# Performance work log

Measured on AMD Instinct MI355X. Metric: run time of the kernel, lower is better.

Reference implementation:

```python
import jax, jax.numpy as jnp
import numpy as np

DIM = 128
NUM_HEADS = 8
HEAD_DIM = DIM // NUM_HEADS
SCALE = HEAD_DIM ** -0.5


def _attn_branch(xs, Wq, bq, Wp, bp):
    # xs: (N, L, C) batch of sequences; Q=K=V=q (per the module)
    N, L, C = xs.shape
    q = xs @ Wq + bq                                   # (N, L, C)
    q = q.reshape(N, L, NUM_HEADS, HEAD_DIM).transpose(0, 2, 1, 3)  # (N, h, L, d)
    qs = q * SCALE
    attn = jax.nn.softmax(jnp.einsum('nhld,nhmd->nhlm', qs, qs), axis=-1)
    out = jnp.einsum('nhlm,nhmd->nhld', attn, q)       # (N, h, L, d)
    out = out.transpose(0, 2, 1, 3).reshape(N, L, C)
    return out @ Wp + bp


def setup_inputs() -> dict:
    key = jax.random.key(0)
    ks = jax.random.split(key, 12)
    B, C, D, H, W = 1, DIM, 31, 32, 32
    s = 0.02
    return {
        'x': jax.random.normal(ks[0], (B, C, D, H, W), jnp.float32),
        'Wq_spec': jax.random.normal(ks[1], (C, C), jnp.float32) * s,
        'bq_spec': jnp.zeros((C,), jnp.float32),
        'Wp_spec': jax.random.normal(ks[2], (C, C), jnp.float32) * s,
        'bp_spec': jnp.zeros((C,), jnp.float32),
        'Wq_spat': jax.random.normal(ks[3], (C, C), jnp.float32) * s,
        'bq_spat': jnp.zeros((C,), jnp.float32),
        'Wp_spat': jax.random.normal(ks[4], (C, C), jnp.float32) * s,
        'bp_spat': jnp.zeros((C,), jnp.float32),
        'Wg': jax.random.normal(ks[5], (2 * C, C), jnp.float32) * s,
        'bg': jnp.zeros((C,), jnp.float32),
    }


def reference(x, Wq_spec, bq_spec, Wp_spec, bp_spec,
              Wq_spat, bq_spat, Wp_spat, bp_spat, Wg, bg):
    B, C, D, H, W = x.shape
    # ---- spectral branch: sequences of length D per spatial position ----
    x_spec = x.transpose(0, 3, 4, 2, 1).reshape(B * H * W, D, C)
    out_spec = _attn_branch(x_spec, Wq_spec, bq_spec, Wp_spec, bp_spec)
    out_spectral = out_spec.reshape(B, H, W, D, C).transpose(0, 4, 3, 1, 2)  # (B,C,D,H,W)
    # ---- spatial branch: sequences of length H*W per band ----
    x_spat = x.transpose(0, 2, 3, 4, 1).reshape(B * D, H * W, C)
    out_spat = _attn_branch(x_spat, Wq_spat, bq_spat, Wp_spat, bp_spat)
    out_spatial = out_spat.reshape(B, D, H, W, C).transpose(0, 4, 1, 2, 3)   # (B,C,D,H,W)
    # ---- sigmoid-gated fusion (global average pooled gate) ----
    gi = jnp.concatenate([
        out_spectral.mean(axis=(2, 3, 4)),
        out_spatial.mean(axis=(2, 3, 4)),
    ], axis=-1)                                          # (B, 2C)
    gate = jax.nn.sigmoid(gi @ Wg + bg)[:, :, None, None, None]  # (B,C,1,1,1)
    return gate * out_spectral + (1.0 - gate) * out_spatial
```

## Files before the change

kernel.cpp:

```cpp
#include <hip/hip_runtime.h>
#include <cstddef>

#define CC 128
#define NH 8
#define HD 16
#define DDIM 31
#define HWW 1024
#define TOK 31744
#define SCALE2 0.0625f
#define QTOK 64

typedef __attribute__((ext_vector_type(4))) short  short4v;
typedef __attribute__((ext_vector_type(8))) short  short8v;
typedef __attribute__((ext_vector_type(4))) float  float4v;
typedef __attribute__((ext_vector_type(2))) unsigned uint2v;
typedef __attribute__((ext_vector_type(8))) __bf16 bf16x8;

__device__ inline unsigned bf16rne(float f) {
    unsigned u = __float_as_uint(f);
    return (u + 0x7fffu + ((u >> 16) & 1u)) >> 16;
}
__device__ inline float bf2f(unsigned h) { return __uint_as_float(h << 16); }

__device__ inline unsigned packsplit(float v) {
    unsigned h = bf16rne(v);
    unsigned l = bf16rne(v - bf2f(h));
    return h | (l << 16);
}
__device__ inline uint2 pack_hi4(uint4 p) {
    return make_uint2((p.x & 0xffffu) | (p.y << 16),
                      (p.z & 0xffffu) | (p.w << 16));
}
__device__ inline uint2 pack_lo4(uint4 p) {
    return make_uint2((p.x >> 16) | (p.y & 0xffff0000u),
                      (p.z >> 16) | (p.w & 0xffff0000u));
}

__device__ inline short4v pack_pf(unsigned u0, unsigned u1,
                                  unsigned u2, unsigned u3) {
    uint2v pd;
    pd[0] = __builtin_amdgcn_perm(u1, u0, 0x07060302u);
    pd[1] = __builtin_amdgcn_perm(u3, u2, 0x07060302u);
    return __builtin_bit_cast(short4v, pd);
}

__device__ inline float4v mfma32(short8v a, short8v b, float4v c) {
    return __builtin_amdgcn_mfma_f32_16x16x32_bf16(
        __builtin_bit_cast(bf16x8, a), __builtin_bit_cast(bf16x8, b), c, 0, 0, 0);
}

__device__ inline void load_wfrags32(const float* __restrict__ W, int co0, int l,
                                     int quad, short8v* ah, short8v* al)
{
#pragma unroll
    for (int k4 = 0; k4 < 4; ++k4) {
#pragma unroll
        for (int j = 0; j < 8; ++j) {
            float w = W[(size_t)(k4 * 32 + quad * 8 + j) * CC + co0 + l];
            unsigned h = bf16rne(w);
            ah[k4][j] = (short)h;
            al[k4][j] = (short)bf16rne(w - bf2f(h));
        }
    }
}

#define AST 136

__global__ __launch_bounds__(512, 4) void qproj_kernel(
    const float* __restrict__ x,
    const float* __restrict__ Wq1, const float* __restrict__ Wq2,
    const float* __restrict__ bq1, const float* __restrict__ bq2,
    unsigned* __restrict__ q1p, unsigned* __restrict__ q2p,
    float* __restrict__ sums)
{
    __shared__ ushort sbuf[2 * QTOK * AST];
    ushort* Ahi = sbuf;
    ushort* Alo = sbuf + QTOK * AST;
    unsigned* S = (unsigned*)sbuf;
    const int tid = threadIdx.x;
    const int t0  = blockIdx.x * QTOK;
    if (blockIdx.x == 0 && tid < 2 * CC) sums[tid] = 0.f;

    for (int i = tid; i < CC * QTOK / 4; i += 512) {
        int t4 = i & 15, ci = i >> 4;
        float4 v = *(const float4*)&x[(size_t)ci * TOK + t0 + t4 * 4];
        float xv[4] = {v.x, v.y, v.z, v.w};
#pragma unroll
        for (int e = 0; e < 4; ++e) {
            unsigned h = bf16rne(xv[e]);
            unsigned lw = bf16rne(xv[e] - bf2f(h));
            Ahi[(t4 * 4 + e) * AST + ci] = (ushort)h;
            Alo[(t4 * 4 + e) * AST + ci] = (ushort)lw;
        }
    }
    __syncthreads();

    const int lane = tid & 63;
    const int l    = lane & 15;
    const int quad = lane >> 4;
    const int co0  = (tid >> 6) * 16;

    short8v ah[2][4], al[2][4];
    load_wfrags32(Wq1, co0, l, quad, ah[0], al[0]);
    load_wfrags32(Wq2, co0, l, quad, ah[1], al[1]);
    float4v acc[2][4];
#pragma unroll
    for (int br = 0; br < 2; ++br)
#pragma unroll
        for (int nt = 0; nt < 4; ++nt) acc[br][nt] = (float4v){0.f, 0.f, 0.f, 0.f};
#pragma unroll
    for (int k4 = 0; k4 < 4; ++k4) {
#pragma unroll
        for (int nt = 0; nt < 4; ++nt) {
            short8v bh = *(const short8v*)&Ahi[(nt * 16 + l) * AST + k4 * 32 + quad * 8];
            short8v bl = *(const short8v*)&Alo[(nt * 16 + l) * AST + k4 * 32 + quad * 8];
            acc[0][nt] = mfma32(ah[0][k4], bh, acc[0][nt]);
            acc[0][nt] = mfma32(ah[0][k4], bl, acc[0][nt]);
            acc[0][nt] = mfma32(al[0][k4], bh, acc[0][nt]);
            acc[1][nt] = mfma32(ah[1][k4], bh, acc[1][nt]);
            acc[1][nt] = mfma32(ah[1][k4], bl, acc[1][nt]);
            acc[1][nt] = mfma32(al[1][k4], bh, acc[1][nt]);
        }
    }

    for (int branch = 0; branch < 2; ++branch) {
        const float* bq = branch ? bq2 : bq1;
        unsigned* op    = branch ? q2p : q1p;
        float4 bv = *(const float4*)&bq[co0 + quad * 4];
        float bb[4] = {bv.x, bv.y, bv.z, bv.w};
        __syncthreads();
#pragma unroll
        for (int nt = 0; nt < 4; ++nt) {
#pragma unroll
            for (int reg = 0; reg < 4; ++reg)
                S[(nt * 16 + l) * AST + co0 + quad * 4 + reg] =
                    packsplit(acc[branch][nt][reg] + bb[reg]);
        }
        __syncthreads();
        for (int i = tid; i < QTOK * 32; i += 512) {
            int t = i >> 5, c4 = i & 31;
            uint4 pv = *(const uint4*)&S[t * AST + c4 * 4];
            *(uint4*)&op[(size_t)(t0 + t) * CC + c4 * 4] = pv;
        }
    }
}

#define QS2 132
#define QSS 20
#define QTP 1044
__global__ __launch_bounds__(1024, 4) void attn_kernel(
    unsigned* __restrict__ q1p, unsigned* __restrict__ q2p,
    float* __restrict__ sums)
{
    __shared__ __align__(16) ushort smem[HWW * QSS + HD * QTP];
    __shared__ float fsum[CC];
    const int tid  = threadIdx.x;
    const int lane = tid & 63;
    const int l    = lane & 15;
    const int quad = lane >> 4;
    const float k2 = SCALE2 * 1.44269504f;
    const short4v onesb = {(short)0x3F80, (short)0x3F80, (short)0x3F80, (short)0x3F80};
    if (tid < CC) fsum[tid] = 0.f;

    {
        const int d = blockIdx.x >> 3, h = blockIdx.x & 7;
        ushort* Qs  = smem;
        ushort* QTs = smem + HWW * QSS;
        const size_t base = (size_t)d * HWW * CC + h * HD;

        for (int i = tid; i < HWW * 4; i += 1024) {
            int row = i >> 2, q4 = i & 3;
            uint4 p = *(const uint4*)&q2p[base + (size_t)row * CC + q4 * 4];
            *(uint2*)&Qs[row * QSS + q4 * 4] = pack_hi4(p);
            QTs[(q4 * 4 + 0) * QTP + row] = (ushort)p.x;
            QTs[(q4 * 4 + 1) * QTP + row] = (ushort)p.y;
            QTs[(q4 * 4 + 2) * QTP + row] = (ushort)p.z;
            QTs[(q4 * 4 + 3) * QTP + row] = (ushort)p.w;
        }
        __syncthreads();

        const int Rw = (tid >> 6) * 64;
        short4v qf[4];
#pragma unroll
        for (int lt = 0; lt < 4; ++lt) {
            short4v raw = *(short4v*)&Qs[(Rw + lt * 16 + l) * QSS + quad * 4];
            short4v sc;
#pragma unroll
            for (int e = 0; e < 4; ++e) {
                float f = bf2f((unsigned)(ushort)raw[e]) * k2;
                sc[e] = (short)bf16rne(f);
            }
            qf[lt] = sc;
        }

        float4v acc[4], accs[4];
#pragma unroll
        for (int lt = 0; lt < 4; ++lt) {
            acc[lt]  = (float4v){0.f, 0.f, 0.f, 0.f};
            accs[lt] = (float4v){0.f, 0.f, 0.f, 0.f};
        }

#pragma unroll 2
        for (int mt = 0; mt < 64; ++mt) {
            const int m0 = mt * 16;
            short4v ka = *(short4v*)&Qs[(m0 + l) * QSS + quad * 4];
            short4v vb = *(short4v*)&QTs[l * QTP + m0 + quad * 4];
#pragma unroll
            for (int lt = 0; lt < 4; ++lt) {
                float4v s = __builtin_amdgcn_mfma_f32_16x16x16bf16_1k(
                    ka, qf[lt], (float4v){0.f, 0.f, 0.f, 0.f}, 0, 0, 0);
                unsigned u0 = __float_as_uint(__builtin_amdgcn_exp2f(s[0]));
                unsigned u1 = __float_as_uint(__builtin_amdgcn_exp2f(s[1]));
                unsigned u2 = __float_as_uint(__builtin_amdgcn_exp2f(s[2]));
                unsigned u3 = __float_as_uint(__builtin_amdgcn_exp2f(s[3]));
                short4v pf = pack_pf(u0, u1, u2, u3);
                acc[lt]  = __builtin_amdgcn_mfma_f32_16x16x16bf16_1k(vb, pf, acc[lt], 0, 0, 0);
                accs[lt] = __builtin_amdgcn_mfma_f32_16x16x16bf16_1k(onesb, pf, accs[lt], 0, 0, 0);
            }
        }

        float vsum[4] = {0.f, 0.f, 0.f, 0.f};
#pragma unroll
        for (int lt = 0; lt < 4; ++lt) {
            float inv = 1.f / accs[lt][0];
            int token = Rw + lt * 16 + l;
            float v0 = acc[lt][0] * inv, v1 = acc[lt][1] * inv;
            float v2 = acc[lt][2] * inv, v3 = acc[lt][3] * inv;
            uint4 pv;
            pv.x = packsplit(v0); pv.y = packsplit(v1);
            pv.z = packsplit(v2); pv.w = packsplit(v3);
            *(uint4*)&q2p[base + (size_t)token * CC + quad * 4] = pv;
            vsum[0] += v0; vsum[1] += v1; vsum[2] += v2; vsum[3] += v3;
        }
#pragma unroll
        for (int reg = 0; reg < 4; ++reg) {
            float v = vsum[reg];
            v += __shfl_xor(v, 1); v += __shfl_xor(v, 2);
            v += __shfl_xor(v, 4); v += __shfl_xor(v, 8);
            if (l == 0) atomicAdd(&fsum[quad * 4 + reg], v);
        }
        __syncthreads();
        if (tid < HD) atomicAdd(&sums[CC + h * HD + tid], fsum[tid]);
    }

    const int half_id = blockIdx.x >> 1;
    const bool has_job = (blockIdx.x & 1) ? (half_id < 4) : (half_id < 124);
    if (!has_job) return;
    const int job = (blockIdx.x & 1) ? (124 + half_id) : half_id;
    const int hw0 = job * 8;

    __syncthreads();
    if (tid < CC) fsum[tid] = 0.f;

    const int wave = tid >> 6;
    const int hwl  = wave >> 1;
    const int half = wave & 1;
    const int hw   = hw0 + hwl;
    ushort* Q = smem + hwl * (32 * QS2);
    for (int it = 0; it < 8; ++it) {
        int idx = it * 64 + lane;
        int dd = half * 16 + (idx >> 5), c4 = idx & 31;
        if (dd < 31) {
            uint4 p = *(const uint4*)&q1p[((size_t)dd * HWW + hw) * CC + c4 * 4];
            *(uint2*)&Q[dd * QS2 + c4 * 4] = pack_hi4(p);
        }
    }
    if (half) for (int i = lane; i < 128; i += 64) Q[31 * QS2 + i] = 0;
    __syncthreads();

    const int hh = half * 4;
#pragma unroll
    for (int hl = 0; hl < 4; ++hl) {
        const int hc = (hh + hl) * HD;
        short4v qf[2];
        qf[0] = *(const short4v*)&Q[l * QS2 + hc + quad * 4];
        qf[1] = *(const short4v*)&Q[(16 + l) * QS2 + hc + quad * 4];
        short4v va[2];
#pragma unroll
        for (int j = 0; j < 2; ++j)
#pragma unroll
            for (int jj = 0; jj < 4; ++jj)
                va[j][jj] = (short)Q[(j * 16 + quad * 4 + jj) * QS2 + hc + l];

        float4v o[2]   = {(float4v){0.f,0.f,0.f,0.f}, (float4v){0.f,0.f,0.f,0.f}};
        float4v osr[2] = {(float4v){0.f,0.f,0.f,0.f}, (float4v){0.f,0.f,0.f,0.f}};
#pragma unroll
        for (int j = 0; j < 2; ++j) {
#pragma unroll
            for (int i2 = 0; i2 < 2; ++i2) {
                float4v s = __builtin_amdgcn_mfma_f32_16x16x16bf16_1k(
                    qf[j], qf[i2], (float4v){0.f,0.f,0.f,0.f}, 0, 0, 0);
                unsigned u0 = __float_as_uint(__builtin_amdgcn_exp2f(s[0] * k2));
                unsigned u1 = __float_as_uint(__builtin_amdgcn_exp2f(s[1] * k2));
                unsigned u2 = __float_as_uint(__builtin_amdgcn_exp2f(s[2] * k2));
                unsigned u3 = __float_as_uint(__builtin_amdgcn_exp2f(s[3] * k2));
                if (j == 1 && quad == 3) u3 = 0;
                short4v pf = pack_pf(u0, u1, u2, u3);
                o[i2]   = __builtin_amdgcn_mfma_f32_16x16x16bf16_1k(va[j], pf, o[i2], 0, 0, 0);
                osr[i2] = __builtin_amdgcn_mfma_f32_16x16x16bf16_1k(onesb, pf, osr[i2], 0, 0, 0);
            }
        }
        float vsum[4] = {0.f, 0.f, 0.f, 0.f};
#pragma unroll
        for (int i2 = 0; i2 < 2; ++i2) {
            float inv = 1.f / osr[i2][0];
            int dq = i2 * 16 + l;
            if (dq < 31) {
                uint4 pv;
                float v0 = o[i2][0] * inv, v1 = o[i2][1] * inv;
                float v2 = o[i2][2] * inv, v3 = o[i2][3] * inv;
                pv.x = packsplit(v0); pv.y = packsplit(v1);
                pv.z = packsplit(v2); pv.w = packsplit(v3);
                *(uint4*)&q1p[((size_t)dq * HWW + hw) * CC + hc + quad * 4] = pv;
                vsum[0] += v0; vsum[1] += v1; vsum[2] += v2; vsum[3] += v3;
            }
        }
#pragma unroll
        for (int r = 0; r < 4; ++r) {
            float v = vsum[r];
            v += __shfl_xor(v, 1); v += __shfl_xor(v, 2);
            v += __shfl_xor(v, 4); v += __shfl_xor(v, 8);
            if (l == 0) atomicAdd(&fsum[hc + quad * 4 + r], v);
        }
    }
    __syncthreads();
    if (tid < CC) atomicAdd(&sums[tid], fsum[tid]);
}

__global__ __launch_bounds__(512, 4) void oproj_kernel(
    const unsigned* __restrict__ q1p, const unsigned* __restrict__ q2p,
    const float* __restrict__ Wp1, const float* __restrict__ Wp2,
    const float* __restrict__ bp1, const float* __restrict__ bp2,
    const float* __restrict__ Wg,  const float* __restrict__ bg,
    const float* __restrict__ sums, float* __restrict__ out)
{
    __shared__ ushort sbuf[2 * 64 * AST];
    ushort* Ahi = sbuf;
    ushort* Alo = sbuf + 64 * AST;
    unsigned* S = (unsigned*)sbuf;
    __shared__ float pa[4][CC];
    __shared__ float giv[2 * CC];
    __shared__ float gf[CC];
    const int tid = threadIdx.x;
    const int t0  = blockIdx.x * 64;
    const int lane = tid & 63;
    const int l    = lane & 15;
    const int quad = lane >> 4;
    const int co0  = (tid >> 6) * 16;

    {
        const int part = tid >> 7, c = tid & 127;
        const float* Wp = (part < 2) ? Wp1 : Wp2;
        const float* sp = (part < 2) ? sums : sums + CC;
        const int k0 = (part & 1) * 64;
        float a = 0.f;
        for (int kk = 0; kk < 64; ++kk) {
            int k = k0 + kk;
            a += sp[k] * Wp[(size_t)k * CC + c];
        }
        pa[part][c] = a;
        __syncthreads();
        if (tid < 2 * CC) {
            float m = (tid < CC) ? (pa[0][tid] + pa[1][tid])
                                 : (pa[2][tid - CC] + pa[3][tid - CC]);
            float bb = (tid < CC) ? bp1[tid] : bp2[tid - CC];
            giv[tid] = m * (1.f / (float)TOK) + bb;
        }
        __syncthreads();
        float b = 0.f;
        for (int kk = 0; kk < 64; ++kk) {
            int j = part * 64 + kk;
            b += giv[j] * Wg[(size_t)j * CC + c];
        }
        pa[part][c] = b;
        __syncthreads();
        if (tid < CC)
            gf[tid] = 1.f / (1.f + __expf(-(bg[tid] + pa[0][tid] + pa[1][tid] +
                                           pa[2][tid] + pa[3][tid])));
    }

    float4v acc[2][4];
#pragma unroll
    for (int br = 0; br < 2; ++br)
#pragma unroll
        for (int nt = 0; nt < 4; ++nt) acc[br][nt] = (float4v){0.f, 0.f, 0.f, 0.f};

    for (int br = 0; br < 2; ++br) {
        const unsigned* Ap = br ? q2p : q1p;
        const float*    W  = br ? Wp2 : Wp1;
        short8v ah[4], al[4];
        load_wfrags32(W, co0, l, quad, ah, al);
        __syncthreads();
        for (int i = tid; i < 64 * 32; i += 512) {
            int t = i >> 5, c4 = i & 31;
            uint4 p = *(const uint4*)&Ap[(size_t)(t0 + t) * CC + c4 * 4];
            *(uint2*)&Ahi[t * AST + c4 * 4] = pack_hi4(p);
            *(uint2*)&Alo[t * AST + c4 * 4] = pack_lo4(p);
        }
        __syncthreads();
#pragma unroll
        for (int k4 = 0; k4 < 4; ++k4) {
#pragma unroll
            for (int nt = 0; nt < 4; ++nt) {
                short8v bh = *(const short8v*)&Ahi[(nt * 16 + l) * AST + k4 * 32 + quad * 8];
                short8v bl = *(const short8v*)&Alo[(nt * 16 + l) * AST + k4 * 32 + quad * 8];
                acc[br][nt] = mfma32(ah[k4], bh, acc[br][nt]);
                acc[br][nt] = mfma32(ah[k4], bl, acc[br][nt]);
                acc[br][nt] = mfma32(al[k4], bh, acc[br][nt]);
            }
        }
    }

    float4 b1 = *(const float4*)&bp1[co0 + quad * 4];
    float4 b2 = *(const float4*)&bp2[co0 + quad * 4];
    float bb1[4] = {b1.x, b1.y, b1.z, b1.w};
    float bb2[4] = {b2.x, b2.y, b2.z, b2.w};
    float gg[4];
#pragma unroll
    for (int e = 0; e < 4; ++e) gg[e] = gf[co0 + quad * 4 + e];

    __syncthreads();
#pragma unroll
    for (int nt = 0; nt < 4; ++nt) {
        int tl = nt * 16 + l;
#pragma unroll
        for (int reg = 0; reg < 4; ++reg) {
            float v = gg[reg] * (acc[0][nt][reg] + bb1[reg]) +
                      (1.f - gg[reg]) * (acc[1][nt][reg] + bb2[reg]);
            S[(co0 + quad * 4 + reg) * 66 + tl] = __float_as_uint(v);
        }
    }
    __syncthreads();
    for (int i = tid; i < 128 * 32; i += 512) {
        int co = i >> 5, t2 = i & 31;
        uint2 v = *(const uint2*)&S[co * 66 + t2 * 2];
        *(uint2*)&out[(size_t)co * TOK + t0 + t2 * 2] = v;
    }
}

extern "C" void kernel_launch(void* const* d_in, const int* in_sizes, int n_in,
                              void* d_out, int out_size, void* d_ws, size_t ws_size,
                              hipStream_t stream)
{
    const float* x   = (const float*)d_in[0];
    const float* Wq1 = (const float*)d_in[1];
    const float* bq1 = (const float*)d_in[2];
    const float* Wp1 = (const float*)d_in[3];
    const float* bp1 = (const float*)d_in[4];
    const float* Wq2 = (const float*)d_in[5];
    const float* bq2 = (const float*)d_in[6];
    const float* Wp2 = (const float*)d_in[7];
    const float* bp2 = (const float*)d_in[8];
    const float* Wg  = (const float*)d_in[9];
    const float* bg  = (const float*)d_in[10];
    float* out = (float*)d_out;

    const size_t plane = (size_t)TOK * CC;
    unsigned* q1p = (unsigned*)d_ws;
    unsigned* q2p = q1p + plane;
    float*   sums = (float*)(q2p + plane);

    qproj_kernel<<<dim3(TOK / QTOK), 512, 0, stream>>>(x, Wq1, Wq2, bq1, bq2,
                                                       q1p, q2p, sums);
    attn_kernel<<<dim3(248), 1024, 0, stream>>>(q1p, q2p, sums);
    oproj_kernel<<<dim3(496), 512, 0, stream>>>(q1p, q2p,
                                                Wp1, Wp2, bp1, bp2, Wg, bg,
                                                sums, out);
}
```

Before: 173.0 us.

## Use 16x16x32 bf16 MFMA for PV and row-sum, coalesce x staging

Both attention kernels now compute two 16-key score tiles and pack the exponentials into an 8-element bf16 fragment. The PV product and the softmax row-sum then run as single K=32 MFMAs instead of pairs of K=16 MFMAs, which halves the accumulation instruction count. The qproj staging loop is also reorganised so each thread loads scalar x values along the token dimension and writes packed 4-channel uint2 words to LDS instead of scattered ushort stores. The trade-off is higher register pressure from keeping two score tiles live, plus a reliance on the K-slot mapping of the 16x16x32 MFMA lining up with the concatenated fragments.

```diff
diff --git a/kernel.cpp b/kernel.cpp
--- a/kernel.cpp
+++ b/kernel.cpp
@@ -14,6 +14,7 @@
 typedef __attribute__((ext_vector_type(8))) short  short8v;
 typedef __attribute__((ext_vector_type(4))) float  float4v;
 typedef __attribute__((ext_vector_type(2))) unsigned uint2v;
+typedef __attribute__((ext_vector_type(4))) unsigned uint4v;
 typedef __attribute__((ext_vector_type(8))) __bf16 bf16x8;
 
 __device__ inline unsigned bf16rne(float f) {
@@ -36,17 +37,24 @@
                       (p.z >> 16) | (p.w & 0xffff0000u));
 }
 
-__device__ inline short4v pack_pf(unsigned u0, unsigned u1,
-                                  unsigned u2, unsigned u3) {
-    uint2v pd;
+__device__ inline short8v pack_pf8(unsigned u0, unsigned u1, unsigned u2,
+                                   unsigned u3, unsigned u4, unsigned u5,
+                                   unsigned u6, unsigned u7) {
+    uint4v pd;
     pd[0] = __builtin_amdgcn_perm(u1, u0, 0x07060302u);
     pd[1] = __builtin_amdgcn_perm(u3, u2, 0x07060302u);
-    return __builtin_bit_cast(short4v, pd);
+    pd[2] = __builtin_amdgcn_perm(u5, u4, 0x07060302u);
+    pd[3] = __builtin_amdgcn_perm(u7, u6, 0x07060302u);
+    return __builtin_bit_cast(short8v, pd);
 }
 
 __device__ inline float4v mfma32(short8v a, short8v b, float4v c) {
     return __builtin_amdgcn_mfma_f32_16x16x32_bf16(
         __builtin_bit_cast(bf16x8, a), __builtin_bit_cast(bf16x8, b), c, 0, 0, 0);
+}
+__device__ inline float4v mfma16(short4v a, short4v b) {
+    return __builtin_amdgcn_mfma_f32_16x16x16bf16_1k(
+        a, b, (float4v){0.f, 0.f, 0.f, 0.f}, 0, 0, 0);
 }
 
 __device__ inline void load_wfrags32(const float* __restrict__ W, int co0, int l,
@@ -81,17 +89,25 @@
     const int t0  = blockIdx.x * QTOK;
     if (blockIdx.x == 0 && tid < 2 * CC) sums[tid] = 0.f;
 
-    for (int i = tid; i < CC * QTOK / 4; i += 512) {
-        int t4 = i & 15, ci = i >> 4;
-        float4 v = *(const float4*)&x[(size_t)ci * TOK + t0 + t4 * 4];
-        float xv[4] = {v.x, v.y, v.z, v.w};
-#pragma unroll
-        for (int e = 0; e < 4; ++e) {
-            unsigned h = bf16rne(xv[e]);
-            unsigned lw = bf16rne(xv[e] - bf2f(h));
-            Ahi[(t4 * 4 + e) * AST + ci] = (ushort)h;
-            Alo[(t4 * 4 + e) * AST + ci] = (ushort)lw;
-        }
+    for (int i = tid; i < QTOK * 32; i += 512) {
+        int t = i & 63, c4 = i >> 6;
+        unsigned hw[2], lw[2];
+#pragma unroll
+        for (int p = 0; p < 2; ++p) {
+            unsigned h0, l0, h1, l1;
+            {
+                float v = x[(size_t)(c4 * 4 + p * 2 + 0) * TOK + t0 + t];
+                h0 = bf16rne(v); l0 = bf16rne(v - bf2f(h0));
+            }
+            {
+                float v = x[(size_t)(c4 * 4 + p * 2 + 1) * TOK + t0 + t];
+                h1 = bf16rne(v); l1 = bf16rne(v - bf2f(h1));
+            }
+            hw[p] = h0 | (h1 << 16);
+            lw[p] = l0 | (l1 << 16);
+        }
+        *(uint2*)&Ahi[t * AST + c4 * 4] = make_uint2(hw[0], hw[1]);
+        *(uint2*)&Alo[t * AST + c4 * 4] = make_uint2(lw[0], lw[1]);
     }
     __syncthreads();
 
@@ -159,7 +175,8 @@
     const int l    = lane & 15;
     const int quad = lane >> 4;
     const float k2 = SCALE2 * 1.44269504f;
-    const short4v onesb = {(short)0x3F80, (short)0x3F80, (short)0x3F80, (short)0x3F80};
+    const short8v ones8 = {(short)0x3F80, (short)0x3F80, (short)0x3F80, (short)0x3F80,
+                           (short)0x3F80, (short)0x3F80, (short)0x3F80, (short)0x3F80};
     if (tid < CC) fsum[tid] = 0.f;
 
     {
@@ -200,22 +217,28 @@
             accs[lt] = (float4v){0.f, 0.f, 0.f, 0.f};
         }
 
-#pragma unroll 2
-        for (int mt = 0; mt < 64; ++mt) {
-            const int m0 = mt * 16;
-            short4v ka = *(short4v*)&Qs[(m0 + l) * QSS + quad * 4];
-            short4v vb = *(short4v*)&QTs[l * QTP + m0 + quad * 4];
+        for (int mt2 = 0; mt2 < 32; ++mt2) {
+            const int m0 = mt2 * 32;
+            short4v ka0 = *(short4v*)&Qs[(m0 + l) * QSS + quad * 4];
+            short4v ka1 = *(short4v*)&Qs[(m0 + 16 + l) * QSS + quad * 4];
+            short4v v0  = *(short4v*)&QTs[l * QTP + m0 + quad * 4];
+            short4v v1  = *(short4v*)&QTs[l * QTP + m0 + 16 + quad * 4];
+            short8v vb  = __builtin_shufflevector(v0, v1, 0, 1, 2, 3, 4, 5, 6, 7);
 #pragma unroll
             for (int lt = 0; lt < 4; ++lt) {
-                float4v s = __builtin_amdgcn_mfma_f32_16x16x16bf16_1k(
-                    ka, qf[lt], (float4v){0.f, 0.f, 0.f, 0.f}, 0, 0, 0);
-                unsigned u0 = __float_as_uint(__builtin_amdgcn_exp2f(s[0]));
-                unsigned u1 = __float_as_uint(__builtin_amdgcn_exp2f(s[1]));
-                unsigned u2 = __float_as_uint(__builtin_amdgcn_exp2f(s[2]));
-                unsigned u3 = __float_as_uint(__builtin_amdgcn_exp2f(s[3]));
-                short4v pf = pack_pf(u0, u1, u2, u3);
-                acc[lt]  = __builtin_amdgcn_mfma_f32_16x16x16bf16_1k(vb, pf, acc[lt], 0, 0, 0);
-                accs[lt] = __builtin_amdgcn_mfma_f32_16x16x16bf16_1k(onesb, pf, accs[lt], 0, 0, 0);
+                float4v s0 = mfma16(ka0, qf[lt]);
+                float4v s1 = mfma16(ka1, qf[lt]);
+                unsigned u0 = __float_as_uint(__builtin_amdgcn_exp2f(s0[0]));
+                unsigned u1 = __float_as_uint(__builtin_amdgcn_exp2f(s0[1]));
+                unsigned u2 = __float_as_uint(__builtin_amdgcn_exp2f(s0[2]));
+                unsigned u3 = __float_as_uint(__builtin_amdgcn_exp2f(s0[3]));
+                unsigned u4 = __float_as_uint(__builtin_amdgcn_exp2f(s1[0]));
+                unsigned u5 = __float_as_uint(__builtin_amdgcn_exp2f(s1[1]));
+                unsigned u6 = __float_as_uint(__builtin_amdgcn_exp2f(s1[2]));
+                unsigned u7 = __float_as_uint(__builtin_amdgcn_exp2f(s1[3]));
+                short8v pf = pack_pf8(u0, u1, u2, u3, u4, u5, u6, u7);
+                acc[lt]  = mfma32(vb, pf, acc[lt]);
+                accs[lt] = mfma32(ones8, pf, accs[lt]);
             }
         }
 
@@ -275,30 +298,31 @@
         short4v qf[2];
         qf[0] = *(const short4v*)&Q[l * QS2 + hc + quad * 4];
         qf[1] = *(const short4v*)&Q[(16 + l) * QS2 + hc + quad * 4];
-        short4v va[2];
-#pragma unroll
-        for (int j = 0; j < 2; ++j)
-#pragma unroll
-            for (int jj = 0; jj < 4; ++jj)
-                va[j][jj] = (short)Q[(j * 16 + quad * 4 + jj) * QS2 + hc + l];
+        short8v va8;
+#pragma unroll
+        for (int jj = 0; jj < 4; ++jj) {
+            va8[jj]     = (short)Q[(quad * 4 + jj) * QS2 + hc + l];
+            va8[jj + 4] = (short)Q[(16 + quad * 4 + jj) * QS2 + hc + l];
+        }
 
         float4v o[2]   = {(float4v){0.f,0.f,0.f,0.f}, (float4v){0.f,0.f,0.f,0.f}};
         float4v osr[2] = {(float4v){0.f,0.f,0.f,0.f}, (float4v){0.f,0.f,0.f,0.f}};
 #pragma unroll
-        for (int j = 0; j < 2; ++j) {
-#pragma unroll
-            for (int i2 = 0; i2 < 2; ++i2) {
-                float4v s = __builtin_amdgcn_mfma_f32_16x16x16bf16_1k(
-                    qf[j], qf[i2], (float4v){0.f,0.f,0.f,0.f}, 0, 0, 0);
-                unsigned u0 = __float_as_uint(__builtin_amdgcn_exp2f(s[0] * k2));
-                unsigned u1 = __float_as_uint(__builtin_amdgcn_exp2f(s[1] * k2));
-                unsigned u2 = __float_as_uint(__builtin_amdgcn_exp2f(s[2] * k2));
-                unsigned u3 = __float_as_uint(__builtin_amdgcn_exp2f(s[3] * k2));
-                if (j == 1 && quad == 3) u3 = 0;
-                short4v pf = pack_pf(u0, u1, u2, u3);
-                o[i2]   = __builtin_amdgcn_mfma_f32_16x16x16bf16_1k(va[j], pf, o[i2], 0, 0, 0);
-                osr[i2] = __builtin_amdgcn_mfma_f32_16x16x16bf16_1k(onesb, pf, osr[i2], 0, 0, 0);
-            }
+        for (int i2 = 0; i2 < 2; ++i2) {
+            float4v s0 = mfma16(qf[0], qf[i2]);
+            float4v s1 = mfma16(qf[1], qf[i2]);
+            unsigned u0 = __float_as_uint(__builtin_amdgcn_exp2f(s0[0] * k2));
+            unsigned u1 = __float_as_uint(__builtin_amdgcn_exp2f(s0[1] * k2));
+            unsigned u2 = __float_as_uint(__builtin_amdgcn_exp2f(s0[2] * k2));
+            unsigned u3 = __float_as_uint(__builtin_amdgcn_exp2f(s0[3] * k2));
+            unsigned u4 = __float_as_uint(__builtin_amdgcn_exp2f(s1[0] * k2));
+            unsigned u5 = __float_as_uint(__builtin_amdgcn_exp2f(s1[1] * k2));
+            unsigned u6 = __float_as_uint(__builtin_amdgcn_exp2f(s1[2] * k2));
+            unsigned u7 = __float_as_uint(__builtin_amdgcn_exp2f(s1[3] * k2));
+            if (quad == 3) u7 = 0;
+            short8v pf = pack_pf8(u0, u1, u2, u3, u4, u5, u6, u7);
+            o[i2]   = mfma32(va8, pf, o[i2]);
+            osr[i2] = mfma32(ones8, pf, osr[i2]);
         }
         float vsum[4] = {0.f, 0.f, 0.f, 0.f};
 #pragma unroll
```

Measured after the change: 170.4 us. About the same (-1.5%).

## Precompute split-bf16 weight planes and hoist gate computation into separate kernels

Applied to the files above, without the earlier changes.

Adds a prep kernel that converts the four projection weight matrices once into hi/lo bf16 planes in the workspace. The qproj and oproj blocks then load MFMA fragments with vector loads instead of each block doing strided fp32 loads and conversions. The sigmoid gate, previously recomputed redundantly by all 496 oproj blocks, moves to a single-block kernel, and the x staging loop in qproj is restructured to write packed pairs to LDS. The cost is two extra kernel launches and a serial dependency on the one-block gate kernel.

```diff
diff --git a/kernel.cpp b/kernel.cpp
--- a/kernel.cpp
+++ b/kernel.cpp
@@ -49,26 +49,53 @@
         __builtin_bit_cast(bf16x8, a), __builtin_bit_cast(bf16x8, b), c, 0, 0, 0);
 }
 
-__device__ inline void load_wfrags32(const float* __restrict__ W, int co0, int l,
-                                     int quad, short8v* ah, short8v* al)
-{
+#define AST 136
+#define WPL (CC * CC)
+
+__global__ __launch_bounds__(256) void wprep_kernel(
+    const float* __restrict__ Wq1, const float* __restrict__ Wq2,
+    const float* __restrict__ Wp1, const float* __restrict__ Wp2,
+    ushort* __restrict__ wplanes)
+{
+    const int m = blockIdx.x >> 4;
+    const int e = (blockIdx.x & 15) * 256 + threadIdx.x;
+    const int co = e >> 5, kb = e & 31;
+    const float* W = (m == 0) ? Wq1 : (m == 1) ? Wq2 : (m == 2) ? Wp1 : Wp2;
+    ushort* hi = wplanes + (size_t)m * 2 * WPL;
+    ushort* lo = hi + WPL;
+    ushort hv[4], lv[4];
+#pragma unroll
+    for (int j = 0; j < 4; ++j) {
+        float w = W[(size_t)(kb * 4 + j) * CC + co];
+        unsigned h = bf16rne(w);
+        hv[j] = (ushort)h;
+        lv[j] = (ushort)bf16rne(w - bf2f(h));
+    }
+    *(uint2*)&hi[(size_t)co * CC + kb * 4] =
+        make_uint2((unsigned)hv[0] | ((unsigned)hv[1] << 16),
+                   (unsigned)hv[2] | ((unsigned)hv[3] << 16));
+    *(uint2*)&lo[(size_t)co * CC + kb * 4] =
+        make_uint2((unsigned)lv[0] | ((unsigned)lv[1] << 16),
+                   (unsigned)lv[2] | ((unsigned)lv[3] << 16));
+}
+
+__device__ inline void load_wfrags_p(const ushort* __restrict__ Whi,
+                                     const ushort* __restrict__ Wlo,
+                                     int co0, int l, int quad,
+                                     short8v* ah, short8v* al)
+{
+    const ushort* rh = Whi + (size_t)(co0 + l) * CC + quad * 8;
+    const ushort* rl = Wlo + (size_t)(co0 + l) * CC + quad * 8;
 #pragma unroll
     for (int k4 = 0; k4 < 4; ++k4) {
-#pragma unroll
-        for (int j = 0; j < 8; ++j) {
-            float w = W[(size_t)(k4 * 32 + quad * 8 + j) * CC + co0 + l];
-            unsigned h = bf16rne(w);
-            ah[k4][j] = (short)h;
-            al[k4][j] = (short)bf16rne(w - bf2f(h));
-        }
-    }
-}
-
-#define AST 136
+        ah[k4] = *(const short8v*)&rh[k4 * 32];
+        al[k4] = *(const short8v*)&rl[k4 * 32];
+    }
+}
 
 __global__ __launch_bounds__(512, 4) void qproj_kernel(
     const float* __restrict__ x,
-    const float* __restrict__ Wq1, const float* __restrict__ Wq2,
+    const ushort* __restrict__ wplanes,
     const float* __restrict__ bq1, const float* __restrict__ bq2,
     unsigned* __restrict__ q1p, unsigned* __restrict__ q2p,
     float* __restrict__ sums)
@@ -81,17 +108,25 @@
     const int t0  = blockIdx.x * QTOK;
     if (blockIdx.x == 0 && tid < 2 * CC) sums[tid] = 0.f;
 
-    for (int i = tid; i < CC * QTOK / 4; i += 512) {
-        int t4 = i & 15, ci = i >> 4;
-        float4 v = *(const float4*)&x[(size_t)ci * TOK + t0 + t4 * 4];
-        float xv[4] = {v.x, v.y, v.z, v.w};
-#pragma unroll
-        for (int e = 0; e < 4; ++e) {
-            unsigned h = bf16rne(xv[e]);
-            unsigned lw = bf16rne(xv[e] - bf2f(h));
-            Ahi[(t4 * 4 + e) * AST + ci] = (ushort)h;
-            Alo[(t4 * 4 + e) * AST + ci] = (ushort)lw;
-        }
+    for (int i = tid; i < QTOK * 32; i += 512) {
+        int t = i & 63, c4 = i >> 6;
+        unsigned hw[2], lw[2];
+#pragma unroll
+        for (int p = 0; p < 2; ++p) {
+            unsigned h0, l0, h1, l1;
+            {
+                float v = x[(size_t)(c4 * 4 + p * 2 + 0) * TOK + t0 + t];
+                h0 = bf16rne(v); l0 = bf16rne(v - bf2f(h0));
+            }
+            {
+                float v = x[(size_t)(c4 * 4 + p * 2 + 1) * TOK + t0 + t];
+                h1 = bf16rne(v); l1 = bf16rne(v - bf2f(h1));
+            }
+            hw[p] = h0 | (h1 << 16);
+            lw[p] = l0 | (l1 << 16);
+        }
+        *(uint2*)&Ahi[t * AST + c4 * 4] = make_uint2(hw[0], hw[1]);
+        *(uint2*)&Alo[t * AST + c4 * 4] = make_uint2(lw[0], lw[1]);
     }
     __syncthreads();
 
@@ -101,8 +136,8 @@
     const int co0  = (tid >> 6) * 16;
 
     short8v ah[2][4], al[2][4];
-    load_wfrags32(Wq1, co0, l, quad, ah[0], al[0]);
-    load_wfrags32(Wq2, co0, l, quad, ah[1], al[1]);
+    load_wfrags_p(wplanes,           wplanes + WPL,     co0, l, quad, ah[0], al[0]);
+    load_wfrags_p(wplanes + 2 * WPL, wplanes + 3 * WPL, co0, l, quad, ah[1], al[1]);
     float4v acc[2][4];
 #pragma unroll
     for (int br = 0; br < 2; ++br)
@@ -327,20 +362,55 @@
     if (tid < CC) atomicAdd(&sums[tid], fsum[tid]);
 }
 
-__global__ __launch_bounds__(512, 4) void oproj_kernel(
-    const unsigned* __restrict__ q1p, const unsigned* __restrict__ q2p,
+__global__ __launch_bounds__(512) void gate_kernel(
     const float* __restrict__ Wp1, const float* __restrict__ Wp2,
     const float* __restrict__ bp1, const float* __restrict__ bp2,
     const float* __restrict__ Wg,  const float* __restrict__ bg,
-    const float* __restrict__ sums, float* __restrict__ out)
+    const float* __restrict__ sums, float* __restrict__ gfp)
+{
+    __shared__ float pa[4][CC];
+    __shared__ float giv[2 * CC];
+    const int tid = threadIdx.x;
+    const int part = tid >> 7, c = tid & 127;
+    const float* Wp = (part < 2) ? Wp1 : Wp2;
+    const float* sp = (part < 2) ? sums : sums + CC;
+    const int k0 = (part & 1) * 64;
+    float a = 0.f;
+    for (int kk = 0; kk < 64; ++kk) {
+        int k = k0 + kk;
+        a += sp[k] * Wp[(size_t)k * CC + c];
+    }
+    pa[part][c] = a;
+    __syncthreads();
+    if (tid < 2 * CC) {
+        float m = (tid < CC) ? (pa[0][tid] + pa[1][tid])
+                             : (pa[2][tid - CC] + pa[3][tid - CC]);
+        float bb = (tid < CC) ? bp1[tid] : bp2[tid - CC];
+        giv[tid] = m * (1.f / (float)TOK) + bb;
+    }
+    __syncthreads();
+    float b = 0.f;
+    for (int kk = 0; kk < 64; ++kk) {
+        int j = part * 64 + kk;
+        b += giv[j] * Wg[(size_t)j * CC + c];
+    }
+    pa[part][c] = b;
+    __syncthreads();
+    if (tid < CC)
+        gfp[tid] = 1.f / (1.f + __expf(-(bg[tid] + pa[0][tid] + pa[1][tid] +
+                                        pa[2][tid] + pa[3][tid])));
+}
+
+__global__ __launch_bounds__(512, 4) void oproj_kernel(
+    const unsigned* __restrict__ q1p, const unsigned* __restrict__ q2p,
+    const ushort* __restrict__ wplanes,
+    const float* __restrict__ bp1, const float* __restrict__ bp2,
+    const float* __restrict__ gfp, float* __restrict__ out)
 {
     __shared__ ushort sbuf[2 * 64 * AST];
     ushort* Ahi = sbuf;
     ushort* Alo = sbuf + 64 * AST;
     unsigned* S = (unsigned*)sbuf;
-    __shared__ float pa[4][CC];
-    __shared__ float giv[2 * CC];
-    __shared__ float gf[CC];
     const int tid = threadIdx.x;
     const int t0  = blockIdx.x * 64;
     const int lane = tid & 63;
@@ -348,37 +418,6 @@
     const int quad = lane >> 4;
     const int co0  = (tid >> 6) * 16;
 
-    {
-        const int part = tid >> 7, c = tid & 127;
-        const float* Wp = (part < 2) ? Wp1 : Wp2;
-        const float* sp = (part < 2) ? sums : sums + CC;
-        const int k0 = (part & 1) * 64;
-        float a = 0.f;
-        for (int kk = 0; kk < 64; ++kk) {
-            int k = k0 + kk;
-            a += sp[k] * Wp[(size_t)k * CC + c];
-        }
-        pa[part][c] = a;
-        __syncthreads();
-        if (tid < 2 * CC) {
-            float m = (tid < CC) ? (pa[0][tid] + pa[1][tid])
-                                 : (pa[2][tid - CC] + pa[3][tid - CC]);
-            float bb = (tid < CC) ? bp1[tid] : bp2[tid - CC];
-            giv[tid] = m * (1.f / (float)TOK) + bb;
-        }
-        __syncthreads();
-        float b = 0.f;
-        for (int kk = 0; kk < 64; ++kk) {
-            int j = part * 64 + kk;
-            b += giv[j] * Wg[(size_t)j * CC + c];
-        }
-        pa[part][c] = b;
-        __syncthreads();
-        if (tid < CC)
-            gf[tid] = 1.f / (1.f + __expf(-(bg[tid] + pa[0][tid] + pa[1][tid] +
-                                           pa[2][tid] + pa[3][tid])));
-    }
-
     float4v acc[2][4];
 #pragma unroll
     for (int br = 0; br < 2; ++br)
@@ -387,10 +426,10 @@
 
     for (int br = 0; br < 2; ++br) {
         const unsigned* Ap = br ? q2p : q1p;
-        const float*    W  = br ? Wp2 : Wp1;
+        const ushort* Whi = wplanes + (size_t)(2 + br) * 2 * WPL;
         short8v ah[4], al[4];
-        load_wfrags32(W, co0, l, quad, ah, al);
-        __syncthreads();
+        load_wfrags_p(Whi, Whi + WPL, co0, l, quad, ah, al);
+        if (br) __syncthreads();
         for (int i = tid; i < 64 * 32; i += 512) {
             int t = i >> 5, c4 = i & 31;
             uint4 p = *(const uint4*)&Ap[(size_t)(t0 + t) * CC + c4 * 4];
@@ -415,9 +454,8 @@
     float4 b2 = *(const float4*)&bp2[co0 + quad * 4];
     float bb1[4] = {b1.x, b1.y, b1.z, b1.w};
     float bb2[4] = {b2.x, b2.y, b2.z, b2.w};
-    float gg[4];
-#pragma unroll
-    for (int e = 0; e < 4; ++e) gg[e] = gf[co0 + quad * 4 + e];
+    float4 gv = *(const float4*)&gfp[co0 + quad * 4];
+    float gg[4] = {gv.x, gv.y, gv.z, gv.w};
 
     __syncthreads();
 #pragma unroll
@@ -459,11 +497,20 @@
     unsigned* q1p = (unsigned*)d_ws;
     unsigned* q2p = q1p + plane;
     float*   sums = (float*)(q2p + plane);
-
-    qproj_kernel<<<dim3(TOK / QTOK), 512, 0, stream>>>(x, Wq1, Wq2, bq1, bq2,
+    float*   gfp  = sums + 2 * CC;
+    ushort*  wpl  = (ushort*)(gfp + CC);
+
+    const size_t need = 2 * plane * sizeof(unsigned) +
+                        (2 * CC + CC) * sizeof(float) +
+                        (size_t)4 * 2 * WPL * sizeof(ushort);
+    if (ws_size < need) return;
+
+    wprep_kernel<<<dim3(64), 256, 0, stream>>>(Wq1, Wq2, Wp1, Wp2, wpl);
+    qproj_kernel<<<dim3(TOK / QTOK), 512, 0, stream>>>(x, wpl, bq1, bq2,
                                                        q1p, q2p, sums);
     attn_kernel<<<dim3(248), 1024, 0, stream>>>(q1p, q2p, sums);
-    oproj_kernel<<<dim3(496), 512, 0, stream>>>(q1p, q2p,
-                                                Wp1, Wp2, bp1, bp2, Wg, bg,
-                                                sums, out);
-}
+    gate_kernel<<<dim3(1), 512, 0, stream>>>(Wp1, Wp2, bp1, bp2, Wg, bg,
+                                             sums, gfp);
+    oproj_kernel<<<dim3(496), 512, 0, stream>>>(q1p, q2p, wpl,
+                                                bp1, bp2, gfp, out);
+}
```

After: 177.0 us. 2.3% more time.
